# Performance work log

Measured on AMD Instinct MI355X. Metric: run time of the kernel, lower is better.

The kernel has to match this reference:

```python
import jax, jax.numpy as jnp
import numpy as np

D = 128  # embedding dim (hardcoded by nn.Linear(128*2, 1))


def setup_inputs() -> dict:
    key = jax.random.key(0)
    k1, k2, k3, k4 = jax.random.split(key, 4)
    B, T, N = 256, 64, 2048
    targetsentence_emb = jax.random.normal(k1, (B, T, D), dtype=jnp.float32)
    context_emb = jax.random.normal(k2, (B, N, D), dtype=jnp.float32)
    # Linear(2D -> 1): weight [1, 2D], bias [1]. Store as flat vectors.
    W = jax.random.normal(k3, (2 * D,), dtype=jnp.float32) * (1.0 / np.sqrt(2 * D))
    b = jax.random.normal(k4, (1,), dtype=jnp.float32) * 0.01
    return {"targetsentence_emb": targetsentence_emb, "context_emb": context_emb, "W": W, "b": b}


def reference(targetsentence_emb, context_emb, W, b):
    # Decompose concat+Linear: W = [Wt | Wc], both length D.
    Wt, Wc = W[:D], W[D:]
    T = targetsentence_emb.shape[1]
    # score[b, n] = sum_t (Wt . target[b,t] + Wc . ctx[b,n] + bias)
    #            = sum_t(Wt . target[b,t]) + T * (Wc . ctx[b,n] + bias)
    tgt_term = jnp.einsum('btd,d->b', targetsentence_emb, Wt)  # [B]
    ctx_term = jnp.einsum('bnd,d->bn', context_emb, Wc)        # [B, N]
    scores = tgt_term[:, None] + T * (ctx_term + b[0])         # [B, N]
    attention = jax.nn.softmax(scores, axis=1)                 # softmax over context dim
    # einsum 'bnm,bnk->bnk' with m=1 is elementwise broadcast scaling
    return attention[:, :, None] * context_emb                 # [B, N, D]
```

## Files before the change

### kernel.cpp

```cpp
#include <hip/hip_runtime.h>


#define B_DIM 256
#define N_DIM 2048
#define D_DIM 128
#define DVEC  (D_DIM / 4)
#define T_SCALE 64.0f

typedef float f4v __attribute__((ext_vector_type(4)));

__global__ __launch_bounds__(256)
void k_scores(const float* __restrict__ ctx, const float* __restrict__ W,
              float* __restrict__ scores) {
    const int tid  = threadIdx.x;
    const int wave = tid >> 6;
    const int lane = tid & 63;
    const int sub  = lane & 31;
    const int half = lane >> 5;
    const int r    = blockIdx.x * 8 + wave * 2 + half;

    const float4 wc = ((const float4*)(W + D_DIM))[sub];
    const float4 v  = ((const float4*)ctx)[(size_t)r * DVEC + sub];
    float p = v.x * wc.x + v.y * wc.y + v.z * wc.z + v.w * wc.w;
    #pragma unroll
    for (int m = 1; m < 32; m <<= 1) p += __shfl_xor(p, m, 64);
    if (sub == 0) scores[r] = T_SCALE * p;
}

__global__ __launch_bounds__(256)
void k_softmax(float* __restrict__ s) {
    const int tid  = threadIdx.x;
    const int wave = tid >> 6;
    const int lane = tid & 63;
    float4* row4 = (float4*)(s + (size_t)blockIdx.x * N_DIM);

    __shared__ float red[4];

    float4 a = row4[tid];
    float4 c = row4[tid + 256];

    float m0 = fmaxf(fmaxf(fmaxf(a.x, a.y), fmaxf(a.z, a.w)),
                     fmaxf(fmaxf(c.x, c.y), fmaxf(c.z, c.w)));
    #pragma unroll
    for (int m = 1; m < 64; m <<= 1) m0 = fmaxf(m0, __shfl_xor(m0, m, 64));
    if (lane == 0) red[wave] = m0;
    __syncthreads();
    const float gmax = fmaxf(fmaxf(red[0], red[1]), fmaxf(red[2], red[3]));
    __syncthreads();

    a.x = __expf(a.x - gmax); a.y = __expf(a.y - gmax);
    a.z = __expf(a.z - gmax); a.w = __expf(a.w - gmax);
    c.x = __expf(c.x - gmax); c.y = __expf(c.y - gmax);
    c.z = __expf(c.z - gmax); c.w = __expf(c.w - gmax);

    float sum = a.x + a.y + a.z + a.w + c.x + c.y + c.z + c.w;
    #pragma unroll
    for (int m = 1; m < 64; m <<= 1) sum += __shfl_xor(sum, m, 64);
    if (lane == 0) red[wave] = sum;
    __syncthreads();
    const float inv = 1.0f / (red[0] + red[1] + red[2] + red[3]);

    a.x *= inv; a.y *= inv; a.z *= inv; a.w *= inv;
    c.x *= inv; c.y *= inv; c.z *= inv; c.w *= inv;
    row4[tid]       = a;
    row4[tid + 256] = c;
}

__global__ __launch_bounds__(256)
void k_scale(const float* __restrict__ ctx, const float* __restrict__ p,
             float* __restrict__ out) {
    const int tid = threadIdx.x;
    const int rb  = gridDim.x - 1 - blockIdx.x;
    const size_t base_row = (size_t)rb * 64;

    __shared__ float sp[64];
    if (tid < 64) sp[tid] = p[base_row + tid];
    __syncthreads();

    const f4v* c4 = (const f4v*)ctx + base_row * DVEC;
    f4v*       o4 = (f4v*)out       + base_row * DVEC;

    #pragma unroll
    for (int i = 0; i < 8; ++i) {
        const int f = i * 256 + tid;
        const float w = sp[f >> 5];
        f4v v = __builtin_nontemporal_load(&c4[f]);
        v *= w;
        __builtin_nontemporal_store(v, &o4[f]);
    }
}

extern "C" void kernel_launch(void* const* d_in, const int* in_sizes, int n_in,
                              void* d_out, int out_size, void* d_ws, size_t ws_size,
                              hipStream_t stream) {
    (void)in_sizes; (void)n_in; (void)out_size; (void)ws_size;
    const float* ctx = (const float*)d_in[1];
    const float* W   = (const float*)d_in[2];
    float* out       = (float*)d_out;
    float* scores    = (float*)d_ws;

    hipLaunchKernelGGL(k_scores,  dim3(B_DIM * N_DIM / 8), dim3(256), 0, stream,
                       ctx, W, scores);
    hipLaunchKernelGGL(k_softmax, dim3(B_DIM),             dim3(256), 0, stream,
                       scores);
    hipLaunchKernelGGL(k_scale,   dim3(B_DIM * N_DIM / 64), dim3(256), 0, stream,
                       ctx, scores, out);
}
```

Measured before the change: 466.3 us.

## Chunk batches for cache reuse and fuse softmax into scaling kernel

Processes the batch in chunks of 64 so context rows read by the score kernel may still be cache-resident when the scaling kernel rereads them, and switches those reads from nontemporal to normal loads. Softmax is fused into the scaling kernel, with each block recomputing the row max and sum from the score row, which removes the separate softmax pass and its score write-back. This trades extra launches and redundant per-block reduction work for less DRAM traffic.

```diff
diff --git a/kernel.cpp b/kernel.cpp
--- a/kernel.cpp
+++ b/kernel.cpp
@@ -1,26 +1,27 @@
 #include <hip/hip_runtime.h>
 
 
-#define B_DIM 256
-#define N_DIM 2048
-#define D_DIM 128
-#define DVEC  (D_DIM / 4)
+#define B_DIM  256
+#define N_DIM  2048
+#define D_DIM  128
+#define DVEC   (D_DIM / 4)
 #define T_SCALE 64.0f
+#define CHUNK  64
 
 typedef float f4v __attribute__((ext_vector_type(4)));
 
 __global__ __launch_bounds__(256)
 void k_scores(const float* __restrict__ ctx, const float* __restrict__ W,
-              float* __restrict__ scores) {
+              float* __restrict__ scores, int row_base) {
     const int tid  = threadIdx.x;
     const int wave = tid >> 6;
     const int lane = tid & 63;
     const int sub  = lane & 31;
     const int half = lane >> 5;
-    const int r    = blockIdx.x * 8 + wave * 2 + half;
+    const size_t r = (size_t)row_base + blockIdx.x * 8 + wave * 2 + half;
 
     const float4 wc = ((const float4*)(W + D_DIM))[sub];
-    const float4 v  = ((const float4*)ctx)[(size_t)r * DVEC + sub];
+    const float4 v  = ((const float4*)ctx)[r * DVEC + sub];
     float p = v.x * wc.x + v.y * wc.y + v.z * wc.z + v.w * wc.w;
     #pragma unroll
     for (int m = 1; m < 32; m <<= 1) p += __shfl_xor(p, m, 64);
@@ -28,17 +29,23 @@
 }
 
 __global__ __launch_bounds__(256)
-void k_softmax(float* __restrict__ s) {
+void k_softmax_scale(const float* __restrict__ ctx,
+                     const float* __restrict__ scores,
+                     float* __restrict__ out, int batch_base) {
     const int tid  = threadIdx.x;
     const int wave = tid >> 6;
     const int lane = tid & 63;
-    float4* row4 = (float4*)(s + (size_t)blockIdx.x * N_DIM);
+    const int rb   = gridDim.x - 1 - blockIdx.x;
+    const int b    = batch_base + (rb >> 5);
+    const int seg  = rb & 31;
+
+    const float* s = scores + (size_t)b * N_DIM;
 
     __shared__ float red[4];
+    __shared__ float sp[64];
 
-    float4 a = row4[tid];
-    float4 c = row4[tid + 256];
-
+    const float4 a = ((const float4*)s)[tid];
+    const float4 c = ((const float4*)s)[tid + 256];
     float m0 = fmaxf(fmaxf(fmaxf(a.x, a.y), fmaxf(a.z, a.w)),
                      fmaxf(fmaxf(c.x, c.y), fmaxf(c.z, c.w)));
     #pragma unroll
@@ -48,44 +55,27 @@
     const float gmax = fmaxf(fmaxf(red[0], red[1]), fmaxf(red[2], red[3]));
     __syncthreads();
 
-    a.x = __expf(a.x - gmax); a.y = __expf(a.y - gmax);
-    a.z = __expf(a.z - gmax); a.w = __expf(a.w - gmax);
-    c.x = __expf(c.x - gmax); c.y = __expf(c.y - gmax);
-    c.z = __expf(c.z - gmax); c.w = __expf(c.w - gmax);
-
-    float sum = a.x + a.y + a.z + a.w + c.x + c.y + c.z + c.w;
+    float sum = __expf(a.x - gmax) + __expf(a.y - gmax)
+              + __expf(a.z - gmax) + __expf(a.w - gmax)
+              + __expf(c.x - gmax) + __expf(c.y - gmax)
+              + __expf(c.z - gmax) + __expf(c.w - gmax);
     #pragma unroll
     for (int m = 1; m < 64; m <<= 1) sum += __shfl_xor(sum, m, 64);
     if (lane == 0) red[wave] = sum;
     __syncthreads();
     const float inv = 1.0f / (red[0] + red[1] + red[2] + red[3]);
 
-    a.x *= inv; a.y *= inv; a.z *= inv; a.w *= inv;
-    c.x *= inv; c.y *= inv; c.z *= inv; c.w *= inv;
-    row4[tid]       = a;
-    row4[tid + 256] = c;
-}
-
-__global__ __launch_bounds__(256)
-void k_scale(const float* __restrict__ ctx, const float* __restrict__ p,
-             float* __restrict__ out) {
-    const int tid = threadIdx.x;
-    const int rb  = gridDim.x - 1 - blockIdx.x;
-    const size_t base_row = (size_t)rb * 64;
-
-    __shared__ float sp[64];
-    if (tid < 64) sp[tid] = p[base_row + tid];
+    if (tid < 64) sp[tid] = __expf(s[seg * 64 + tid] - gmax) * inv;
     __syncthreads();
 
+    const size_t base_row = (size_t)b * N_DIM + seg * 64;
     const f4v* c4 = (const f4v*)ctx + base_row * DVEC;
     f4v*       o4 = (f4v*)out       + base_row * DVEC;
-
     #pragma unroll
     for (int i = 0; i < 8; ++i) {
         const int f = i * 256 + tid;
-        const float w = sp[f >> 5];
-        f4v v = __builtin_nontemporal_load(&c4[f]);
-        v *= w;
+        f4v v = c4[f];
+        v *= sp[f >> 5];
         __builtin_nontemporal_store(v, &o4[f]);
     }
 }
@@ -99,10 +89,12 @@
     float* out       = (float*)d_out;
     float* scores    = (float*)d_ws;
 
-    hipLaunchKernelGGL(k_scores,  dim3(B_DIM * N_DIM / 8), dim3(256), 0, stream,
-                       ctx, W, scores);
-    hipLaunchKernelGGL(k_softmax, dim3(B_DIM),             dim3(256), 0, stream,
-                       scores);
-    hipLaunchKernelGGL(k_scale,   dim3(B_DIM * N_DIM / 64), dim3(256), 0, stream,
-                       ctx, scores, out);
+    for (int c = 0; c < B_DIM / CHUNK; ++c) {
+        const int batch_base = c * CHUNK;
+        const int row_base   = batch_base * N_DIM;
+        hipLaunchKernelGGL(k_scores, dim3(CHUNK * N_DIM / 8), dim3(256), 0,
+                           stream, ctx, W, scores, row_base);
+        hipLaunchKernelGGL(k_softmax_scale, dim3(CHUNK * 32), dim3(256), 0,
+                           stream, ctx, scores, out, batch_base);
+    }
 }
```

After: 480.2 us. 3.0% more time.
